# Kernel optimization log

Hardware: AMD Instinct MI355X
Metric: run time of the kernel (lower is better)

Reference implementation:

```python
import jax, jax.numpy as jnp
import numpy as np


def _lstm_cell(x, h, c, w_ih, w_hh, b_ih, b_hh):
    gates = x @ w_ih.T + b_ih + h @ w_hh.T + b_hh  # [B, 4H]
    i, f, g, o = jnp.split(gates, 4, axis=1)
    i = jax.nn.sigmoid(i)
    f = jax.nn.sigmoid(f)
    g = jnp.tanh(g)
    o = jax.nn.sigmoid(o)
    c_next = f * c + i * g
    h_next = o * jnp.tanh(c_next)
    return h_next, c_next


def setup_inputs() -> dict:
    key = jax.random.key(0)
    B, T, D_ENC, H, E, J, V = 32, 512, 512, 640, 640, 640, 4096
    ks = jax.random.split(key, 20)
    s = 0.05
    return {
        "encoder_outputs": jax.random.normal(ks[0], (B, D_ENC, T), jnp.float32),
        "targets": jax.random.randint(ks[1], (B, 1), 0, V, jnp.int64),
        "target_length": jnp.ones((B,), jnp.int32),
        "input_states_1": jax.random.normal(ks[2], (2, B, H), jnp.float32),
        "input_states_2": jax.random.normal(ks[3], (2, B, H), jnp.float32),
        "lstm_w_ih_l0": jax.random.normal(ks[4], (4 * H, E), jnp.float32) * s,
        "lstm_w_hh_l0": jax.random.normal(ks[5], (4 * H, H), jnp.float32) * s,
        "lstm_b_ih_l0": jax.random.normal(ks[6], (4 * H,), jnp.float32) * s,
        "lstm_b_hh_l0": jax.random.normal(ks[7], (4 * H,), jnp.float32) * s,
        "lstm_w_ih_l1": jax.random.normal(ks[8], (4 * H, H), jnp.float32) * s,
        "lstm_w_hh_l1": jax.random.normal(ks[9], (4 * H, H), jnp.float32) * s,
        "lstm_b_ih_l1": jax.random.normal(ks[10], (4 * H,), jnp.float32) * s,
        "lstm_b_hh_l1": jax.random.normal(ks[11], (4 * H,), jnp.float32) * s,
        "embed_weight": jax.random.normal(ks[12], (V, E), jnp.float32) * s,
        "joint_enc_weight": jax.random.normal(ks[13], (J, D_ENC), jnp.float32) * s,
        "joint_enc_bias": jax.random.normal(ks[14], (J,), jnp.float32) * s,
        "joint_pred_weight": jax.random.normal(ks[15], (J, H), jnp.float32) * s,
        "joint_pred_bias": jax.random.normal(ks[16], (J,), jnp.float32) * s,
        "joint_out_weight": jax.random.normal(ks[17], (V, J), jnp.float32) * s,
        "joint_out_bias": jax.random.normal(ks[18], (V,), jnp.float32) * s,
    }


def reference(encoder_outputs, targets, target_length, input_states_1, input_states_2,
              lstm_w_ih_l0, lstm_w_hh_l0, lstm_b_ih_l0, lstm_b_hh_l0,
              lstm_w_ih_l1, lstm_w_hh_l1, lstm_b_ih_l1, lstm_b_hh_l1,
              embed_weight, joint_enc_weight, joint_enc_bias,
              joint_pred_weight, joint_pred_bias, joint_out_weight, joint_out_bias):
    tokens = targets.astype(jnp.int64)
    x_t = embed_weight[tokens[:, 0]]  # [B, E] (only first token used)
    h0, c0 = _lstm_cell(x_t, input_states_1[0], input_states_2[0],
                        lstm_w_ih_l0, lstm_w_hh_l0, lstm_b_ih_l0, lstm_b_hh_l0)
    h1, c1 = _lstm_cell(h0, input_states_1[1], input_states_2[1],
                        lstm_w_ih_l1, lstm_w_hh_l1, lstm_b_ih_l1, lstm_b_hh_l1)
    enc = jnp.transpose(encoder_outputs, (0, 2, 1))  # [B, T, D_enc]
    f = enc @ joint_enc_weight.T + joint_enc_bias    # [B, T, J]
    g = h1 @ joint_pred_weight.T + joint_pred_bias   # [B, J] (U=1)
    joint = jax.nn.relu(f[:, :, None, :] + g[:, None, None, :])  # [B, T, 1, J]
    outputs = joint @ joint_out_weight.T + joint_out_bias        # [B, T, 1, V]
    output_states_1 = jnp.stack([h0, h1], axis=0)
    output_states_2 = jnp.stack([c0, c1], axis=0)
    return outputs, target_length, output_states_1, output_states_2
```

## Files before the change

kernel.cpp:

```cpp
#include <hip/hip_runtime.h>
#include <stdint.h>

#define B_  32
#define T_  512
#define DE_ 512
#define H_  640
#define V_  4096
#define J_  640

typedef __attribute__((ext_vector_type(4))) float  f32x4;
typedef __attribute__((ext_vector_type(8))) __bf16 bf16x8;

typedef __attribute__((address_space(3))) void LdsV;
typedef __attribute__((address_space(1))) void GloV;

__device__ __forceinline__ unsigned short f2bf(float f) {
    uint32_t u = __builtin_bit_cast(uint32_t, f);
    u += 0x7fffu + ((u >> 16) & 1u);
    return (unsigned short)(u >> 16);
}

__global__ void conv_f32_bf16_k(const float* __restrict__ src,
                                unsigned short* __restrict__ dst, int n) {
    int i = blockIdx.x * blockDim.x + threadIdx.x;
    if (i < n) dst[i] = f2bf(src[i]);
}

__global__ void enc_transpose_k(const float* __restrict__ enc,
                                unsigned short* __restrict__ out) {
    __shared__ float tile[32][33];
    int b  = blockIdx.z;
    int t0 = blockIdx.x * 32, d0 = blockIdx.y * 32;
    int tx = threadIdx.x & 31;
    int ty = (threadIdx.x >> 5) * 4;
    const float* src = enc + ((size_t)b * DE_ + d0) * T_ + t0;
#pragma unroll
    for (int i = 0; i < 4; i++)
        tile[ty + i][tx] = src[(size_t)(ty + i) * T_ + tx];
    __syncthreads();
    unsigned short* dst = out + ((size_t)b * T_ + t0) * DE_ + d0;
#pragma unroll
    for (int i = 0; i < 4; i++)
        dst[(size_t)(ty + i) * DE_ + tx] = f2bf(tile[tx][ty + i]);
}

__global__ void lstm_gates_k(const float* __restrict__ x, const int* __restrict__ tok,
                             const float* __restrict__ emb, const float* __restrict__ h,
                             const float* __restrict__ wih, const float* __restrict__ whh,
                             const float* __restrict__ bih, const float* __restrict__ bhh,
                             float* __restrict__ gates) {
    int n = blockIdx.x, lane = threadIdx.x;
    float wi[10], wh[10];
#pragma unroll
    for (int i = 0; i < 10; i++) {
        wi[i] = wih[(size_t)n * H_ + lane + 64 * i];
        wh[i] = whh[(size_t)n * H_ + lane + 64 * i];
    }
    float bias = bih[n] + bhh[n];
    for (int b = 0; b < B_; b++) {
        const float* xr = tok ? (emb + (size_t)tok[b] * H_) : (x + (size_t)b * H_);
        const float* hr = h + (size_t)b * H_;
        float s = 0.f;
#pragma unroll
        for (int i = 0; i < 10; i++)
            s += wi[i] * xr[lane + 64 * i] + wh[i] * hr[lane + 64 * i];
#pragma unroll
        for (int off = 32; off > 0; off >>= 1)
            s += __shfl_down(s, off, 64);
        if (lane == 0) gates[(size_t)b * (4 * H_) + n] = s + bias;
    }
}

__global__ void lstm_update_k(const float* __restrict__ gates, const float* __restrict__ c_in,
                              float* __restrict__ h_out, float* __restrict__ c_out,
                              const int* __restrict__ tlen, float* __restrict__ tlen_out) {
    int idx = blockIdx.x * blockDim.x + threadIdx.x;
    if (tlen_out != nullptr && idx < B_) tlen_out[idx] = (float)tlen[idx];
    if (idx >= B_ * H_) return;
    int b = idx / H_, j = idx - b * H_;
    const float* gr = gates + (size_t)b * 4 * H_;
    float ig = 1.f / (1.f + expf(-gr[j]));
    float fg = 1.f / (1.f + expf(-gr[H_ + j]));
    float gg = tanhf(gr[2 * H_ + j]);
    float og = 1.f / (1.f + expf(-gr[3 * H_ + j]));
    float c  = fg * c_in[idx] + ig * gg;
    h_out[idx] = og * tanhf(c);
    c_out[idx] = c;
}

__global__ void pred_g_k(const float* __restrict__ h1, const float* __restrict__ wp,
                         const float* __restrict__ bp, float* __restrict__ g) {
    int j = blockIdx.x, lane = threadIdx.x;
    float w[10];
#pragma unroll
    for (int i = 0; i < 10; i++) w[i] = wp[(size_t)j * H_ + lane + 64 * i];
    for (int b = 0; b < B_; b++) {
        const float* hr = h1 + (size_t)b * H_;
        float s = 0.f;
#pragma unroll
        for (int i = 0; i < 10; i++) s += w[i] * hr[lane + 64 * i];
#pragma unroll
        for (int off = 32; off > 0; off >>= 1)
            s += __shfl_down(s, off, 64);
        if (lane == 0) g[(size_t)b * J_ + j] = s + bp[j];
    }
}

template <int K, int EPI>
__global__ __launch_bounds__(256) void gemm_bt_k(
        const unsigned short* __restrict__ A, const unsigned short* __restrict__ Bm,
        const float* __restrict__ bias, const float* __restrict__ g,
        float* __restrict__ outF, unsigned short* __restrict__ outU, int ldn) {
    __shared__ __align__(16) unsigned short As[128 * 32];
    __shared__ __align__(16) unsigned short Bs[128 * 32];
    const int tid  = threadIdx.x;
    const int w    = tid >> 6;
    const int lane = tid & 63;
    const int tile_n = blockIdx.x * 128;
    const int tile_m = blockIdx.y * 128;
    const int wm = w & 1, wn = w >> 1;
    const int l15 = lane & 15, quad = lane >> 4;
    const int lr = lane >> 2, lc = lane & 3;

    f32x4 zero = {0.f, 0.f, 0.f, 0.f};
    f32x4 acc[4][4];
#pragma unroll
    for (int i = 0; i < 4; i++)
#pragma unroll
        for (int j = 0; j < 4; j++) acc[i][j] = zero;

    for (int k0 = 0; k0 < K; k0 += 32) {
#pragma unroll
        for (int cc = 0; cc < 2; cc++) {
            const int c = 2 * w + cc;
            const char* ga = (const char*)(A + (size_t)(tile_m + 16 * c + lr) * K)
                             + (size_t)k0 * 2 + lc * 16;
            __builtin_amdgcn_global_load_lds((const GloV*)ga,
                    (LdsV*)((char*)As + c * 1024), 16, 0, 0);
            const char* gb = (const char*)(Bm + (size_t)(tile_n + 16 * c + lr) * K)
                             + (size_t)k0 * 2 + lc * 16;
            __builtin_amdgcn_global_load_lds((const GloV*)gb,
                    (LdsV*)((char*)Bs + c * 1024), 16, 0, 0);
        }
        __syncthreads();

        bf16x8 av[4], bv[4];
#pragma unroll
        for (int i = 0; i < 4; i++) {
            av[i] = *(const bf16x8*)&As[(wm * 64 + i * 16 + l15) * 32 + quad * 8];
            bv[i] = *(const bf16x8*)&Bs[(wn * 64 + i * 16 + l15) * 32 + quad * 8];
        }
#pragma unroll
        for (int i = 0; i < 4; i++)
#pragma unroll
            for (int j = 0; j < 4; j++)
                acc[i][j] = __builtin_amdgcn_mfma_f32_16x16x32_bf16(av[i], bv[j], acc[i][j], 0, 0, 0);
        __syncthreads();
    }

#pragma unroll
    for (int i = 0; i < 4; i++) {
        const int mb = tile_m + wm * 64 + i * 16 + quad * 4;
#pragma unroll
        for (int j = 0; j < 4; j++) {
            const int n = tile_n + wn * 64 + j * 16 + l15;
#pragma unroll
            for (int r = 0; r < 4; r++) {
                float v = acc[i][j][r] + bias[n];
                if (EPI == 0) {
                    outF[(size_t)(mb + r) * ldn + n] = v;
                } else {
                    v += g[(size_t)((mb + r) >> 9) * J_ + n];
                    outU[(size_t)(mb + r) * ldn + n] = f2bf(fmaxf(v, 0.f));
                }
            }
        }
    }
}

extern "C" void kernel_launch(void* const* d_in, const int* in_sizes, int n_in,
                              void* d_out, int out_size, void* d_ws, size_t ws_size,
                              hipStream_t stream) {
    const float* enc   = (const float*)d_in[0];
    const int*   tgt   = (const int*)d_in[1];
    const int*   tlen  = (const int*)d_in[2];
    const float* st1   = (const float*)d_in[3];
    const float* st2   = (const float*)d_in[4];
    const float* wih0  = (const float*)d_in[5];
    const float* whh0  = (const float*)d_in[6];
    const float* bih0  = (const float*)d_in[7];
    const float* bhh0  = (const float*)d_in[8];
    const float* wih1  = (const float*)d_in[9];
    const float* whh1  = (const float*)d_in[10];
    const float* bih1  = (const float*)d_in[11];
    const float* bhh1  = (const float*)d_in[12];
    const float* emb   = (const float*)d_in[13];
    const float* wenc  = (const float*)d_in[14];
    const float* benc  = (const float*)d_in[15];
    const float* wpred = (const float*)d_in[16];
    const float* bpred = (const float*)d_in[17];
    const float* wout  = (const float*)d_in[18];
    const float* bout  = (const float*)d_in[19];

    float* out      = (float*)d_out;
    float* out_tlen = out + (size_t)B_ * T_ * V_;
    float* h0 = out_tlen + B_;
    float* h1 = h0 + B_ * H_;
    float* c0 = h1 + B_ * H_;
    float* c1 = c0 + B_ * H_;

    unsigned short* encB  = (unsigned short*)d_ws;
    unsigned short* pB    = encB + (size_t)B_ * T_ * DE_;
    unsigned short* woutB = pB + (size_t)B_ * T_ * J_;
    unsigned short* wencB = woutB + (size_t)V_ * J_;
    float* gates = (float*)(wencB + (size_t)J_ * DE_);
    float* gvec  = gates + B_ * 4 * H_;

    conv_f32_bf16_k<<<(V_ * J_ + 255) / 256, 256, 0, stream>>>(wout, woutB, V_ * J_);
    conv_f32_bf16_k<<<(J_ * DE_ + 255) / 256, 256, 0, stream>>>(wenc, wencB, J_ * DE_);
    enc_transpose_k<<<dim3(T_ / 32, DE_ / 32, B_), 256, 0, stream>>>(enc, encB);

    lstm_gates_k<<<4 * H_, 64, 0, stream>>>(nullptr, tgt, emb, st1, wih0, whh0, bih0, bhh0, gates);
    lstm_update_k<<<(B_ * H_ + 255) / 256, 256, 0, stream>>>(gates, st2, h0, c0, tlen, out_tlen);
    lstm_gates_k<<<4 * H_, 64, 0, stream>>>(h0, nullptr, nullptr, st1 + B_ * H_, wih1, whh1, bih1, bhh1, gates);
    lstm_update_k<<<(B_ * H_ + 255) / 256, 256, 0, stream>>>(gates, st2 + B_ * H_, h1, c1, nullptr, nullptr);
    pred_g_k<<<J_, 64, 0, stream>>>(h1, wpred, bpred, gvec);

    gemm_bt_k<DE_, 1><<<dim3(J_ / 128, (B_ * T_) / 128), 256, 0, stream>>>(
        encB, wencB, benc, gvec, nullptr, pB, J_);
    gemm_bt_k<J_, 0><<<dim3(V_ / 128, (B_ * T_) / 128), 256, 0, stream>>>(
        pB, woutB, bout, nullptr, out, nullptr, V_);
}
```

Before: 536.5 us.

## Replace output GEMM with 256x256-tiled direct-to-LDS double-buffered MFMA kernel

Adds a new bf16 GEMM kernel for the large joint-output projection (16384x4096x640). It uses 256x256 tiles with 512 threads, global_load_lds async copies into double-buffered swizzled LDS, and register prefetch of A fragments across MFMA phases. It also applies a block-index swizzle for L2 locality and s_setprio around the MFMA bursts. The aim is higher arithmetic intensity and overlap of loads with compute than the previous 128x128 kernel, at the cost of 128KB of LDS per block and heavy register pressure.

After: 531.9 us. Within noise of the previous version (-0.8%).

```diff
diff --git a/kernel.cpp b/kernel.cpp
--- a/kernel.cpp
+++ b/kernel.cpp
@@ -19,6 +19,8 @@
     u += 0x7fffu + ((u >> 16) & 1u);
     return (unsigned short)(u >> 16);
 }
+
+__device__ __forceinline__ void sbar() { asm volatile("s_barrier" ::: "memory"); }
 
 __global__ void conv_f32_bf16_k(const float* __restrict__ src,
                                 unsigned short* __restrict__ dst, int n) {
@@ -176,6 +178,134 @@
             }
         }
     }
+}
+
+template <int M, int N, int K>
+__global__ __launch_bounds__(512, 2) void gemm256_k(
+        const unsigned short* __restrict__ A, const unsigned short* __restrict__ Bm,
+        const float* __restrict__ bias, float* __restrict__ out) {
+    __shared__ __align__(16) char lds[131072];
+    constexpr int NT  = K / 64;
+    constexpr int K2  = K * 2;
+    constexpr int NTN = N / 256;
+    constexpr int NWG = (M / 256) * NTN;
+
+    const int bid = blockIdx.x;
+    const int swz = (bid & 7) * (NWG / 8) + (bid >> 3);
+    const int tile_n = (swz % NTN) * 256;
+    const int tile_m = (swz / NTN) * 256;
+
+    const int tid  = threadIdx.x;
+    const int w    = tid >> 6;
+    const int l    = tid & 63;
+    const int wm   = w >> 2;
+    const int wn   = w & 3;
+    const int l15  = l & 15, quad = l >> 4;
+
+    const int lrow = l >> 3;
+    const int lcc  = (l & 7) ^ lrow;
+    const char* gA[4];
+    const char* gB[4];
+    int blk[4];
+#pragma unroll
+    for (int q = 0; q < 4; q++) {
+        blk[q] = (q >> 1) * 16 + w * 2 + (q & 1);
+        gA[q] = (const char*)A  + (size_t)(tile_m + blk[q] * 8 + lrow) * K2 + lcc * 16;
+        gB[q] = (const char*)Bm + (size_t)(tile_n + blk[q] * 8 + lrow) * K2 + lcc * 16;
+    }
+    auto stage = [&](int kt) {
+        char* la = lds + (kt & 1) * 32768;
+        char* lb = lds + 65536 + (kt & 1) * 32768;
+        const int kb = kt * 128;
+#pragma unroll
+        for (int q = 0; q < 4; q++)
+            __builtin_amdgcn_global_load_lds((const GloV*)(gA[q] + kb),
+                    (LdsV*)(la + blk[q] * 1024), 16, 0, 0);
+#pragma unroll
+        for (int q = 0; q < 4; q++)
+            __builtin_amdgcn_global_load_lds((const GloV*)(gB[q] + kb),
+                    (LdsV*)(lb + blk[q] * 1024), 16, 0, 0);
+    };
+
+    const int colk0 = (quad * 16) ^ ((l15 & 7) << 4);
+    const int colk1 = colk0 ^ 64;
+    const int arow  = (wm * 128 + l15) * 128;
+    const int brow  = (wn * 64 + l15) * 128;
+
+    f32x4 acc[8][4];
+    f32x4 zero = {0.f, 0.f, 0.f, 0.f};
+#pragma unroll
+    for (int i = 0; i < 8; i++)
+#pragma unroll
+        for (int j = 0; j < 4; j++) acc[i][j] = zero;
+
+    stage(0);
+    stage(1);
+    asm volatile("s_waitcnt vmcnt(8)" ::: "memory");
+    sbar();
+
+    for (int t = 0; t < NT; ++t) {
+        const char* la = lds + (t & 1) * 32768;
+        const char* lb = lds + 65536 + (t & 1) * 32768;
+
+        bf16x8 bv[2][4];
+#pragma unroll
+        for (int j = 0; j < 4; j++) {
+            bv[0][j] = *(const bf16x8*)(lb + brow + j * 2048 + colk0);
+            bv[1][j] = *(const bf16x8*)(lb + brow + j * 2048 + colk1);
+        }
+        bf16x8 ap[2][2][2];
+        ap[0][0][0] = *(const bf16x8*)(la + arow + 0 * 2048 + colk0);
+        ap[0][0][1] = *(const bf16x8*)(la + arow + 0 * 2048 + colk1);
+        ap[0][1][0] = *(const bf16x8*)(la + arow + 1 * 2048 + colk0);
+        ap[0][1][1] = *(const bf16x8*)(la + arow + 1 * 2048 + colk1);
+
+#pragma unroll
+        for (int ph = 0; ph < 4; ph++) {
+            const int cur = ph & 1, nxt = cur ^ 1;
+            if (ph < 3) {
+                ap[nxt][0][0] = *(const bf16x8*)(la + arow + (2 * ph + 2) * 2048 + colk0);
+                ap[nxt][0][1] = *(const bf16x8*)(la + arow + (2 * ph + 2) * 2048 + colk1);
+                ap[nxt][1][0] = *(const bf16x8*)(la + arow + (2 * ph + 3) * 2048 + colk0);
+                ap[nxt][1][1] = *(const bf16x8*)(la + arow + (2 * ph + 3) * 2048 + colk1);
+            }
+            __builtin_amdgcn_s_setprio(1);
+#pragma unroll
+            for (int ii = 0; ii < 2; ii++)
+#pragma unroll
+                for (int j = 0; j < 4; j++) {
+                    acc[2 * ph + ii][j] = __builtin_amdgcn_mfma_f32_16x16x32_bf16(
+                            ap[cur][ii][0], bv[0][j], acc[2 * ph + ii][j], 0, 0, 0);
+                    acc[2 * ph + ii][j] = __builtin_amdgcn_mfma_f32_16x16x32_bf16(
+                            ap[cur][ii][1], bv[1][j], acc[2 * ph + ii][j], 0, 0, 0);
+                }
+            __builtin_amdgcn_s_setprio(0);
+        }
+
+        sbar();
+        if (t + 2 < NT) {
+            stage(t + 2);
+            asm volatile("s_waitcnt vmcnt(8)" ::: "memory");
+        } else {
+            asm volatile("s_waitcnt vmcnt(0)" ::: "memory");
+        }
+        sbar();
+    }
+
+    const int cb = tile_n + wn * 64 + l15;
+    float bj[4];
+#pragma unroll
+    for (int j = 0; j < 4; j++) bj[j] = bias[cb + j * 16];
+    const int r0 = tile_m + wm * 128 + quad * 4;
+#pragma unroll
+    for (int i = 0; i < 8; i++)
+#pragma unroll
+        for (int r = 0; r < 4; r++) {
+            float* orow = out + (size_t)(r0 + i * 16 + r) * N;
+#pragma unroll
+            for (int j = 0; j < 4; j++)
+                orow[cb + j * 16] = acc[i][j][r] + bj[j];
+        }
 }
 
 extern "C" void kernel_launch(void* const* d_in, const int* in_sizes, int n_in,
@@ -228,6 +358,7 @@
 
     gemm_bt_k<DE_, 1><<<dim3(J_ / 128, (B_ * T_) / 128), 256, 0, stream>>>(
         encB, wencB, benc, gvec, nullptr, pB, J_);
-    gemm_bt_k<J_, 0><<<dim3(V_ / 128, (B_ * T_) / 128), 256, 0, stream>>>(
-        pB, woutB, bout, nullptr, out, nullptr, V_);
-}
+
+    gemm256_k<B_ * T_, V_, J_><<<dim3((B_ * T_ / 256) * (V_ / 256)), 512, 0, stream>>>(
+        pB, woutB, bout, out);
+}
```
